# Performance work log

Hardware: AMD Instinct MI355X
Metric: run time of the kernel (lower is better)

The kernel has to match this reference:

```python
import jax, jax.numpy as jnp
import numpy as np

B, S, H, I, SI, E, TOPK = 2, 1024, 1024, 512, 2048, 8, 2


def setup_inputs() -> dict:
    key = jax.random.key(0)
    ks = jax.random.split(key, 8)
    w = 0.02
    return {
        "hidden_states": jax.random.normal(ks[0], (B, S, H), jnp.float32),
        "router_weight": jax.random.normal(ks[1], (E, H), jnp.float32) * w,
        "gate_up_proj": jax.random.normal(ks[2], (E, 2 * I, H), jnp.float32) * w,
        "down_proj": jax.random.normal(ks[3], (E, H, I), jnp.float32) * w,
        "shared_gate_w": jax.random.normal(ks[4], (SI, H), jnp.float32) * w,
        "shared_up_w": jax.random.normal(ks[5], (SI, H), jnp.float32) * w,
        "shared_down_w": jax.random.normal(ks[6], (H, SI), jnp.float32) * w,
        "shared_expert_gate_w": jax.random.normal(ks[7], (1, H), jnp.float32) * w,
    }


def reference(hidden_states, router_weight, gate_up_proj, down_proj,
              shared_gate_w, shared_up_w, shared_down_w, shared_expert_gate_w):
    b, s, h = hidden_states.shape
    x = hidden_states.reshape(-1, h)  # [T, H]

    # shared expert (SwiGLU)
    shared = (jax.nn.silu(x @ shared_gate_w.T) * (x @ shared_up_w.T)) @ shared_down_w.T  # [T, H]

    # top-k softmax router (softmax in fp32, renormalized top-k weights)
    logits = x @ router_weight.T  # [T, E]
    probs = jax.nn.softmax(logits.astype(jnp.float32), axis=-1)
    top_v, top_i = jax.lax.top_k(probs, TOPK)
    top_v = (top_v / jnp.sum(top_v, axis=-1, keepdims=True)).astype(logits.dtype)  # [T, K]

    # combine weights per (token, expert): sum over k of routing weight * one_hot
    cw = jnp.sum(jax.nn.one_hot(top_i, E, dtype=top_v.dtype) * top_v[..., None], axis=1)  # [T, E]

    # grouped-expert SwiGLU (dense compute, masked combine == gather/scatter math)
    gu = jnp.einsum('th,eih->eti', x, gate_up_proj)  # [E, T, 2I]
    gate, up = jnp.split(gu, 2, axis=-1)
    act = jax.nn.silu(gate) * up  # [E, T, I]
    per_expert = jnp.einsum('eti,ehi->eth', act, down_proj)  # [E, T, H]
    expert_out = jnp.einsum('eth,te->th', per_expert, cw)  # [T, H]

    out = expert_out + jax.nn.sigmoid(x @ shared_expert_gate_w.T) * shared
    return out.reshape(b, s, h)
```

## Files before the change

### kernel.cpp

```cpp
#include <hip/hip_runtime.h>

#define T_TOK 2048
#define H_DIM 1024
#define I_DIM 512
#define SI_DIM 2048
#define E_NUM 8
#define NSLOT 4096

typedef __attribute__((ext_vector_type(8))) short short8;
typedef __attribute__((ext_vector_type(4))) float floatx4;

__device__ inline unsigned short f2bf(float f) {
  unsigned u = __builtin_bit_cast(unsigned, f);
  u = (u + 0x7FFFu + ((u >> 16) & 1u)) >> 16;
  return (unsigned short)u;
}
__device__ inline float bf2f(unsigned short u) {
  return __builtin_bit_cast(float, (unsigned)u << 16);
}

__device__ inline void gl_lds16(const void* g, void* l) {
  __builtin_amdgcn_global_load_lds(
      (const __attribute__((address_space(1))) unsigned int*)g,
      (__attribute__((address_space(3))) unsigned int*)l, 16, 0, 0);
}

__global__ void cast_all(const float* __restrict__ s0, const float* __restrict__ s1,
                         const float* __restrict__ s2, const float* __restrict__ s3,
                         const float* __restrict__ s4, const float* __restrict__ s5,
                         unsigned short* __restrict__ d0, unsigned short* __restrict__ d1,
                         unsigned short* __restrict__ d2, unsigned short* __restrict__ d3,
                         unsigned short* __restrict__ d4, unsigned short* __restrict__ d5) {
  long g = (long)blockIdx.x * blockDim.x + threadIdx.x;
  const float* s;
  unsigned short* d;
  long off;
  if (g < 524288L)       { s = s0; d = d0; off = g; }
  else if (g < 2621440L) { s = s1; d = d1; off = g - 524288L; }
  else if (g < 3670016L) { s = s2; d = d2; off = g - 2621440L; }
  else if (g < 4194304L) { s = s3; d = d3; off = g - 3670016L; }
  else if (g < 4718592L) { s = s4; d = d4; off = g - 4194304L; }
  else                   { s = s5; d = d5; off = g - 4718592L; }
  float4 v = ((const float4*)s)[off];
  ushort4 o;
  o.x = f2bf(v.x); o.y = f2bf(v.y); o.z = f2bf(v.z); o.w = f2bf(v.w);
  ((ushort4*)d)[off] = o;
}

__global__ void router_kernel(const float* __restrict__ x,
                              const float* __restrict__ rw,
                              const float* __restrict__ segw,
                              int* __restrict__ top2,
                              float2* __restrict__ w01,
                              float* __restrict__ sg) {
  int t = blockIdx.x * 4 + (threadIdx.x >> 6);
  int lane = threadIdx.x & 63;
  const float* xt = x + (long)t * H_DIM;
  float xv[16];
#pragma unroll
  for (int j = 0; j < 16; ++j) xv[j] = xt[j * 64 + lane];
  float dots[9];
#pragma unroll
  for (int e = 0; e < 8; ++e) {
    const float* w = rw + e * H_DIM;
    float s = 0.f;
#pragma unroll
    for (int j = 0; j < 16; ++j) s += xv[j] * w[j * 64 + lane];
    dots[e] = s;
  }
  {
    float s = 0.f;
#pragma unroll
    for (int j = 0; j < 16; ++j) s += xv[j] * segw[j * 64 + lane];
    dots[8] = s;
  }
#pragma unroll
  for (int off = 32; off > 0; off >>= 1) {
#pragma unroll
    for (int e = 0; e < 9; ++e) dots[e] += __shfl_xor(dots[e], off, 64);
  }
  if (lane == 0) {
    int e0 = 0;
    for (int e = 1; e < 8; ++e)
      if (dots[e] > dots[e0]) e0 = e;
    int e1 = (e0 == 0) ? 1 : 0;
    for (int e = 0; e < 8; ++e)
      if (e != e0 && dots[e] > dots[e1]) e1 = e;
    float p1 = expf(dots[e1] - dots[e0]);
    float w0 = 1.f / (1.f + p1);
    float w1 = p1 / (1.f + p1);
    top2[t] = e0 | (e1 << 8);
    w01[t] = make_float2(w0, w1);
    sg[t] = 1.f / (1.f + expf(-dots[8]));
  }
}

__global__ __launch_bounds__(256) void build_lists(
    const int* __restrict__ top2, int* __restrict__ cnt, int* __restrict__ ebase,
    int* __restrict__ slot_token, int* __restrict__ tok_slot) {
  const int e = blockIdx.x;
  const int tid = threadIdx.x;
  const int lane = tid & 63, wid = tid >> 6;
  __shared__ int wsum[4], wbelow[4];
  const int base_t = tid * 8;
  int mk[8], kk[8];
  int c = 0, below = 0;
#pragma unroll
  for (int j = 0; j < 8; ++j) {
    int p = top2[base_t + j];
    int e0 = p & 0xFF, e1 = (p >> 8) & 0xFF;
    below += (e0 < e) + (e1 < e);
    int m = 0, k = 0;
    if (e0 == e) { m = 1; k = 0; }
    else if (e1 == e) { m = 1; k = 1; }
    mk[j] = m; kk[j] = k;
    c += m;
  }
  int inc = c;
#pragma unroll
  for (int off = 1; off < 64; off <<= 1) {
    int n = __shfl_up(inc, off, 64);
    if (lane >= off) inc += n;
  }
  int bsum = below;
#pragma unroll
  for (int off = 32; off > 0; off >>= 1) bsum += __shfl_xor(bsum, off, 64);
  if (lane == 63) wsum[wid] = inc;
  if (lane == 0) wbelow[wid] = bsum;
  __syncthreads();
  int woff = 0;
#pragma unroll
  for (int i = 0; i < 4; ++i)
    if (i < wid) woff += wsum[i];
  int baseE = wbelow[0] + wbelow[1] + wbelow[2] + wbelow[3];
  int pos = baseE + woff + inc - c;
#pragma unroll
  for (int j = 0; j < 8; ++j) {
    if (mk[j]) {
      slot_token[pos] = base_t + j;
      tok_slot[2 * (base_t + j) + kk[j]] = pos;
      pos++;
    }
  }
  if (tid == 255) cnt[e] = woff + inc;
  if (tid == 0) ebase[e] = baseE;
}

template <bool GATHER, int BM>
__device__ __forceinline__ void swiglu_body(
    char* smem, int bx, int by, int e,
    const unsigned short* __restrict__ A, const unsigned short* __restrict__ Bg,
    const unsigned short* __restrict__ Bu, unsigned short* __restrict__ Out,
    const int* __restrict__ slot_token, const int* __restrict__ cnt,
    const int* __restrict__ ebase, int N, int K, long estrideB) {
  const int BK = 32;
  const int MT = BM / 32;
  const int ACH = BM / 64;
  const int tid = threadIdx.x;
  const int lane = tid & 63;
  const int wid = tid >> 6;
  const int wm = wid & 1;
  const int wn = wid >> 1;
  const int m0 = by * BM;
  const int n0 = bx * 64;
  int Meff = 0, baseE = 0;
  if (GATHER) {
    Meff = cnt[e];
    if (m0 >= Meff) return;
    baseE = ebase[e];
  }
  const unsigned short* BgE = Bg + (long)e * estrideB;
  const unsigned short* BuE = Bu + (long)e * estrideB;

  unsigned short* As = (unsigned short*)smem;
  unsigned short* Bgs = As + 2 * BM * BK;
  unsigned short* Bus = Bgs + 2 * 64 * BK;

  const int lrow = lane >> 2;
  const int lcol = (((lane & 3) ^ ((lrow >> 1) & 3)) << 4);

  const char* aP[ACH];
#pragma unroll
  for (int i = 0; i < ACH; ++i) {
    int m = m0 + wid * (16 * ACH) + i * 16 + lrow;
    long row;
    if (GATHER) {
      int mm = (m < Meff - 1) ? m : (Meff - 1);
      row = slot_token[baseE + mm];
    } else {
      row = m;
    }
    aP[i] = (const char*)A + row * (long)(K * 2) + lcol;
  }
  int nb = n0 + wid * 16 + lrow;
  const char* bgP = (const char*)BgE + (long)nb * (K * 2) + lcol;
  const char* buP = (const char*)BuE + (long)nb * (K * 2) + lcol;

  floatx4 accG[MT][2], accU[MT][2];
  floatx4 zero = {0.f, 0.f, 0.f, 0.f};
#pragma unroll
  for (int i = 0; i < MT; ++i)
#pragma unroll
    for (int j = 0; j < 2; ++j) { accG[i][j] = zero; accU[i][j] = zero; }

  const int ar = lane & 15;
  const int aksw = (((lane >> 4) ^ ((ar >> 1) & 3)) << 3);

  auto stage = [&](int p, int k0) {
#pragma unroll
    for (int i = 0; i < ACH; ++i)
      gl_lds16(aP[i] + (long)k0 * 2, &As[p * BM * BK + (wid * 16 * ACH + i * 16) * BK]);
    gl_lds16(bgP + (long)k0 * 2, &Bgs[p * 64 * BK + (wid * 16) * BK]);
    gl_lds16(buP + (long)k0 * 2, &Bus[p * 64 * BK + (wid * 16) * BK]);
  };

  stage(0, 0);
  const int NI = K / BK;
  for (int i = 0; i < NI; ++i) {
    __syncthreads();
    if (i + 1 < NI) stage((i + 1) & 1, (i + 1) * BK);
    const unsigned short* Ab = &As[(i & 1) * BM * BK];
    const unsigned short* Gb = &Bgs[(i & 1) * 64 * BK];
    const unsigned short* Ub = &Bus[(i & 1) * 64 * BK];
    short8 af[MT], bgf[2], buf2[2];
#pragma unroll
    for (int tm = 0; tm < MT; ++tm)
      af[tm] = *(const short8*)&Ab[(wm * (BM / 2) + tm * 16 + ar) * BK + aksw];
#pragma unroll
    for (int tn = 0; tn < 2; ++tn) {
      bgf[tn] = *(const short8*)&Gb[(wn * 32 + tn * 16 + ar) * BK + aksw];
      buf2[tn] = *(const short8*)&Ub[(wn * 32 + tn * 16 + ar) * BK + aksw];
    }
#pragma unroll
    for (int tm = 0; tm < MT; ++tm)
#pragma unroll
      for (int tn = 0; tn < 2; ++tn) {
        accG[tm][tn] = __builtin_amdgcn_mfma_f32_16x16x32_bf16(af[tm], bgf[tn], accG[tm][tn], 0, 0, 0);
        accU[tm][tn] = __builtin_amdgcn_mfma_f32_16x16x32_bf16(af[tm], buf2[tn], accU[tm][tn], 0, 0, 0);
      }
  }

#pragma unroll
  for (int tm = 0; tm < MT; ++tm)
#pragma unroll
    for (int tn = 0; tn < 2; ++tn)
#pragma unroll
      for (int r = 0; r < 4; ++r) {
        int row = m0 + wm * (BM / 2) + tm * 16 + (lane >> 4) * 4 + r;
        int col = n0 + wn * 32 + tn * 16 + (lane & 15);
        if (!GATHER || row < Meff) {
          float g = accG[tm][tn][r];
          float u = accU[tm][tn][r];
          float act = g / (1.f + expf(-g)) * u;
          Out[(long)(baseE + row) * N + col] = f2bf(act);
        }
      }
}

__global__ __launch_bounds__(256, 2) void swiglu_fused(
    const unsigned short* __restrict__ xb, const unsigned short* __restrict__ sgate,
    const unsigned short* __restrict__ sup, unsigned short* __restrict__ act_s,
    const unsigned short* __restrict__ gup, unsigned short* __restrict__ act_e,
    const int* __restrict__ slot_token, const int* __restrict__ cnt,
    const int* __restrict__ ebase) {
  __shared__ __align__(16) char smem[32768];
  int bid = blockIdx.x;
  if (bid < 512) {
    swiglu_body<false, 128>(smem, bid & 31, bid >> 5, 0, xb, sgate, sup, act_s,
                            nullptr, nullptr, nullptr, SI_DIM, H_DIM, 0);
  } else {
    int b2 = bid - 512;
    int e = b2 >> 8;
    int rem = b2 & 255;
    swiglu_body<true, 64>(smem, rem & 7, rem >> 3, e, xb, gup,
                          gup + (long)I_DIM * H_DIM, act_e, slot_token, cnt,
                          ebase, I_DIM, H_DIM, (long)2 * I_DIM * H_DIM);
  }
}

template <int MODE>
__device__ __forceinline__ void down_body(
    char* smem, int bx, int by, int e,
    const unsigned short* __restrict__ A, const unsigned short* __restrict__ B,
    float* __restrict__ OutF, unsigned short* __restrict__ OutB,
    const float* __restrict__ sg, const int* __restrict__ ebase,
    const int* __restrict__ cnt, int N, int K, long estrideB) {
  const int BM = 64, BK = 32;
  const int tid = threadIdx.x;
  const int lane = tid & 63;
  const int wid = tid >> 6;
  const int wm = wid & 1;
  const int wn = wid >> 1;
  const int m0 = by * BM;
  const int n0 = bx * 64;
  int Meff = 0, baseE = 0;
  if (MODE == 1) {
    Meff = cnt[e];
    if (m0 >= Meff) return;
    baseE = ebase[e];
  }
  const unsigned short* BE = B + (long)e * estrideB;

  unsigned short* As = (unsigned short*)smem;
  unsigned short* Bs = As + 2 * 64 * BK;

  const int lrow = lane >> 2;
  const int lcol = (((lane & 3) ^ ((lrow >> 1) & 3)) << 4);

  int m = m0 + wid * 16 + lrow;
  long arow;
  if (MODE == 1) {
    int mm = (m < Meff - 1) ? m : (Meff - 1);
    arow = baseE + mm;
  } else {
    arow = m;
  }
  const char* aP = (const char*)A + arow * (long)(K * 2) + lcol;
  int nb = n0 + wid * 16 + lrow;
  const char* bP = (const char*)BE + (long)nb * (K * 2) + lcol;

  floatx4 acc[2][2];
  floatx4 zero = {0.f, 0.f, 0.f, 0.f};
#pragma unroll
  for (int i = 0; i < 2; ++i)
#pragma unroll
    for (int j = 0; j < 2; ++j) acc[i][j] = zero;

  const int ar = lane & 15;
  const int aksw = (((lane >> 4) ^ ((ar >> 1) & 3)) << 3);

  auto stage = [&](int p, int k0) {
    gl_lds16(aP + (long)k0 * 2, &As[p * 64 * BK + (wid * 16) * BK]);
    gl_lds16(bP + (long)k0 * 2, &Bs[p * 64 * BK + (wid * 16) * BK]);
  };

  stage(0, 0);
  const int NI = K / BK;
  for (int i = 0; i < NI; ++i) {
    __syncthreads();
    if (i + 1 < NI) stage((i + 1) & 1, (i + 1) * BK);
    const unsigned short* Ab = &As[(i & 1) * 64 * BK];
    const unsigned short* Bb = &Bs[(i & 1) * 64 * BK];
    short8 af[2], bf[2];
#pragma unroll
    for (int tm = 0; tm < 2; ++tm)
      af[tm] = *(const short8*)&Ab[(wm * 32 + tm * 16 + ar) * BK + aksw];
#pragma unroll
    for (int tn = 0; tn < 2; ++tn)
      bf[tn] = *(const short8*)&Bb[(wn * 32 + tn * 16 + ar) * BK + aksw];
#pragma unroll
    for (int tm = 0; tm < 2; ++tm)
#pragma unroll
      for (int tn = 0; tn < 2; ++tn)
        acc[tm][tn] = __builtin_amdgcn_mfma_f32_16x16x32_bf16(af[tm], bf[tn], acc[tm][tn], 0, 0, 0);
  }

#pragma unroll
  for (int tm = 0; tm < 2; ++tm)
#pragma unroll
    for (int r = 0; r < 4; ++r) {
      int row = m0 + wm * 32 + tm * 16 + (lane >> 4) * 4 + r;
#pragma unroll
      for (int tn = 0; tn < 2; ++tn) {
        int col = n0 + wn * 32 + tn * 16 + (lane & 15);
        float v = acc[tm][tn][r];
        if (MODE == 0) {
          OutF[(long)row * N + col] = sg[row] * v;
        } else if (row < Meff) {
          OutB[(long)(baseE + row) * N + col] = f2bf(v);
        }
      }
    }
}

__global__ __launch_bounds__(256, 4) void down_fused(
    const unsigned short* __restrict__ act_s, const unsigned short* __restrict__ sdown,
    float* __restrict__ out, const float* __restrict__ sg,
    const unsigned short* __restrict__ act_e, const unsigned short* __restrict__ downw,
    unsigned short* __restrict__ eout, const int* __restrict__ ebase,
    const int* __restrict__ cnt) {
  __shared__ __align__(16) char smem[16384];
  int bid = blockIdx.x;
  if (bid < 512) {
    down_body<0>(smem, bid & 15, bid >> 4, 0, act_s, sdown, out, nullptr, sg,
                 nullptr, nullptr, H_DIM, SI_DIM, 0);
  } else {
    int b2 = bid - 512;
    int e = b2 >> 9;
    int rem = b2 & 511;
    down_body<1>(smem, rem & 15, rem >> 4, e, act_e, downw, nullptr, eout,
                 nullptr, ebase, cnt, H_DIM, I_DIM, (long)H_DIM * I_DIM);
  }
}

__global__ __launch_bounds__(256) void combine_kernel(
    float* __restrict__ out, const unsigned short* __restrict__ eout,
    const float2* __restrict__ w01, const int* __restrict__ tok_slot) {
  int t = blockIdx.x;
  int c = threadIdx.x;
  float2 wr = w01[t];
  int s0 = tok_slot[2 * t];
  int s1 = tok_slot[2 * t + 1];
  ushort4 e0 = ((const ushort4*)(eout + (long)s0 * H_DIM))[c];
  ushort4 e1 = ((const ushort4*)(eout + (long)s1 * H_DIM))[c];
  float4* op = &((float4*)(out + (long)t * H_DIM))[c];
  float4 o = *op;
  o.x += wr.x * bf2f(e0.x) + wr.y * bf2f(e1.x);
  o.y += wr.x * bf2f(e0.y) + wr.y * bf2f(e1.y);
  o.z += wr.x * bf2f(e0.z) + wr.y * bf2f(e1.z);
  o.w += wr.x * bf2f(e0.w) + wr.y * bf2f(e1.w);
  *op = o;
}

extern "C" void kernel_launch(void* const* d_in, const int* in_sizes, int n_in,
                              void* d_out, int out_size, void* d_ws, size_t ws_size,
                              hipStream_t stream) {
  const float* x = (const float*)d_in[0];
  const float* rw = (const float*)d_in[1];
  const float* gup = (const float*)d_in[2];
  const float* dwn = (const float*)d_in[3];
  const float* sgw = (const float*)d_in[4];
  const float* suw = (const float*)d_in[5];
  const float* sdw = (const float*)d_in[6];
  const float* segw = (const float*)d_in[7];
  float* out = (float*)d_out;

  char* w = (char*)d_ws;
  unsigned short* xb = (unsigned short*)(w + 0);
  unsigned short* gup_b = (unsigned short*)(w + 4194304L);
  unsigned short* down_b = (unsigned short*)(w + 20971520L);
  unsigned short* sgate_b = (unsigned short*)(w + 29360128L);
  unsigned short* sup_b = (unsigned short*)(w + 33554432L);
  unsigned short* sdown_b = (unsigned short*)(w + 37748736L);
  unsigned short* act_s = (unsigned short*)(w + 41943040L);
  unsigned short* act_e = (unsigned short*)(w + 50331648L);
  unsigned short* eout = (unsigned short*)(w + 54525952L);
  float* sg = (float*)(w + 62914560L);
  int* top2 = (int*)(w + 62922752L);
  float2* w01 = (float2*)(w + 62930944L);
  int* cnt = (int*)(w + 62947328L);
  int* ebase = (int*)(w + 62947584L);
  int* slot_token = (int*)(w + 62947840L);
  int* tok_slot = (int*)(w + 62964224L);

  cast_all<<<20480, 256, 0, stream>>>(x, gup, dwn, sgw, suw, sdw, xb, gup_b,
                                      down_b, sgate_b, sup_b, sdown_b);
  router_kernel<<<512, 256, 0, stream>>>(x, rw, segw, top2, w01, sg);
  build_lists<<<E_NUM, 256, 0, stream>>>(top2, cnt, ebase, slot_token, tok_slot);
  swiglu_fused<<<2560, 256, 0, stream>>>(xb, sgate_b, sup_b, act_s, gup_b,
                                         act_e, slot_token, cnt, ebase);
  down_fused<<<4608, 256, 0, stream>>>(act_s, sdown_b, out, sg, act_e, down_b,
                                       eout, ebase, cnt);
  combine_kernel<<<T_TOK, 256, 0, stream>>>(out, eout, w01, tok_slot);
}
```

Baseline: 218.0 us.

## Merge cast and router kernels, enlarge GEMM tiles, split-K shared down projection

Merges the weight/activation cast and router into one launch, removing a kernel boundary. Grows the expert gate/up tile to 128 rows and the down-projection tile to 128x128, giving fewer blocks and more reuse per LDS load. The shared down GEMM is split in K into two halves: one writes fp32 into the output and the other writes a bf16 partial into the reused x buffer. Combine then sums the halves and applies the sigmoid gate. The larger tiles raise register pressure and lower occupancy (launch bounds drop to 2), and the bf16 partial adds a rounding step.

```diff
diff --git a/kernel.cpp b/kernel.cpp
--- a/kernel.cpp
+++ b/kernel.cpp
@@ -25,73 +25,71 @@
       (__attribute__((address_space(3))) unsigned int*)l, 16, 0, 0);
 }
 
-__global__ void cast_all(const float* __restrict__ s0, const float* __restrict__ s1,
-                         const float* __restrict__ s2, const float* __restrict__ s3,
-                         const float* __restrict__ s4, const float* __restrict__ s5,
-                         unsigned short* __restrict__ d0, unsigned short* __restrict__ d1,
-                         unsigned short* __restrict__ d2, unsigned short* __restrict__ d3,
-                         unsigned short* __restrict__ d4, unsigned short* __restrict__ d5) {
-  long g = (long)blockIdx.x * blockDim.x + threadIdx.x;
-  const float* s;
-  unsigned short* d;
-  long off;
-  if (g < 524288L)       { s = s0; d = d0; off = g; }
-  else if (g < 2621440L) { s = s1; d = d1; off = g - 524288L; }
-  else if (g < 3670016L) { s = s2; d = d2; off = g - 2621440L; }
-  else if (g < 4194304L) { s = s3; d = d3; off = g - 3670016L; }
-  else if (g < 4718592L) { s = s4; d = d4; off = g - 4194304L; }
-  else                   { s = s5; d = d5; off = g - 4718592L; }
-  float4 v = ((const float4*)s)[off];
-  ushort4 o;
-  o.x = f2bf(v.x); o.y = f2bf(v.y); o.z = f2bf(v.z); o.w = f2bf(v.w);
-  ((ushort4*)d)[off] = o;
-}
-
-__global__ void router_kernel(const float* __restrict__ x,
-                              const float* __restrict__ rw,
-                              const float* __restrict__ segw,
-                              int* __restrict__ top2,
-                              float2* __restrict__ w01,
-                              float* __restrict__ sg) {
-  int t = blockIdx.x * 4 + (threadIdx.x >> 6);
-  int lane = threadIdx.x & 63;
-  const float* xt = x + (long)t * H_DIM;
-  float xv[16];
-#pragma unroll
-  for (int j = 0; j < 16; ++j) xv[j] = xt[j * 64 + lane];
-  float dots[9];
-#pragma unroll
-  for (int e = 0; e < 8; ++e) {
-    const float* w = rw + e * H_DIM;
-    float s = 0.f;
-#pragma unroll
-    for (int j = 0; j < 16; ++j) s += xv[j] * w[j * 64 + lane];
-    dots[e] = s;
-  }
-  {
-    float s = 0.f;
-#pragma unroll
-    for (int j = 0; j < 16; ++j) s += xv[j] * segw[j * 64 + lane];
-    dots[8] = s;
-  }
-#pragma unroll
-  for (int off = 32; off > 0; off >>= 1) {
-#pragma unroll
-    for (int e = 0; e < 9; ++e) dots[e] += __shfl_xor(dots[e], off, 64);
-  }
-  if (lane == 0) {
-    int e0 = 0;
-    for (int e = 1; e < 8; ++e)
-      if (dots[e] > dots[e0]) e0 = e;
-    int e1 = (e0 == 0) ? 1 : 0;
-    for (int e = 0; e < 8; ++e)
-      if (e != e0 && dots[e] > dots[e1]) e1 = e;
-    float p1 = expf(dots[e1] - dots[e0]);
-    float w0 = 1.f / (1.f + p1);
-    float w1 = p1 / (1.f + p1);
-    top2[t] = e0 | (e1 << 8);
-    w01[t] = make_float2(w0, w1);
-    sg[t] = 1.f / (1.f + expf(-dots[8]));
+__global__ __launch_bounds__(256) void cast_router(
+    const float* __restrict__ x, const float* __restrict__ rw,
+    const float* __restrict__ segw,
+    const float* __restrict__ s1, const float* __restrict__ s2,
+    const float* __restrict__ s3, const float* __restrict__ s4,
+    const float* __restrict__ s5,
+    unsigned short* __restrict__ d0, unsigned short* __restrict__ d1,
+    unsigned short* __restrict__ d2, unsigned short* __restrict__ d3,
+    unsigned short* __restrict__ d4, unsigned short* __restrict__ d5,
+    int* __restrict__ top2, float2* __restrict__ w01, float* __restrict__ sg) {
+  const int bid = blockIdx.x;
+  if (bid < 512) {
+    int t = bid * 4 + (threadIdx.x >> 6);
+    int lane = threadIdx.x & 63;
+    const float* xt = x + (long)t * H_DIM;
+    float xv[16];
+#pragma unroll
+    for (int j = 0; j < 16; ++j) xv[j] = xt[j * 64 + lane];
+    float dots[9];
+#pragma unroll
+    for (int e = 0; e < 8; ++e) {
+      const float* w = rw + e * H_DIM;
+      float s = 0.f;
+#pragma unroll
+      for (int j = 0; j < 16; ++j) s += xv[j] * w[j * 64 + lane];
+      dots[e] = s;
+    }
+    {
+      float s = 0.f;
+#pragma unroll
+      for (int j = 0; j < 16; ++j) s += xv[j] * segw[j * 64 + lane];
+      dots[8] = s;
+    }
+#pragma unroll
+    for (int off = 32; off > 0; off >>= 1) {
+#pragma unroll
+      for (int e = 0; e < 9; ++e) dots[e] += __shfl_xor(dots[e], off, 64);
+    }
+    if (lane == 0) {
+      int e0 = 0;
+      for (int e = 1; e < 8; ++e)
+        if (dots[e] > dots[e0]) e0 = e;
+      int e1 = (e0 == 0) ? 1 : 0;
+      for (int e = 0; e < 8; ++e)
+        if (e != e0 && dots[e] > dots[e1]) e1 = e;
+      float p1 = expf(dots[e1] - dots[e0]);
+      top2[t] = e0 | (e1 << 8);
+      w01[t] = make_float2(1.f / (1.f + p1), p1 / (1.f + p1));
+      sg[t] = 1.f / (1.f + expf(-dots[8]));
+    }
+  } else {
+    long g = (long)(bid - 512) * 256 + threadIdx.x;
+    const float* s;
+    unsigned short* d;
+    long off;
+    if (g < 524288L)       { s = x;  d = d0; off = g; }
+    else if (g < 2621440L) { s = s1; d = d1; off = g - 524288L; }
+    else if (g < 3670016L) { s = s2; d = d2; off = g - 2621440L; }
+    else if (g < 4194304L) { s = s3; d = d3; off = g - 3670016L; }
+    else if (g < 4718592L) { s = s4; d = d4; off = g - 4194304L; }
+    else                   { s = s5; d = d5; off = g - 4718592L; }
+    float4 v = ((const float4*)s)[off];
+    ushort4 o;
+    o.x = f2bf(v.x); o.y = f2bf(v.y); o.z = f2bf(v.z); o.w = f2bf(v.w);
+    ((ushort4*)d)[off] = o;
   }
 }
 
@@ -146,16 +144,14 @@
   if (tid == 0) ebase[e] = baseE;
 }
 
-template <bool GATHER, int BM>
+template <bool GATHER>
 __device__ __forceinline__ void swiglu_body(
     char* smem, int bx, int by, int e,
     const unsigned short* __restrict__ A, const unsigned short* __restrict__ Bg,
     const unsigned short* __restrict__ Bu, unsigned short* __restrict__ Out,
     const int* __restrict__ slot_token, const int* __restrict__ cnt,
     const int* __restrict__ ebase, int N, int K, long estrideB) {
-  const int BK = 32;
-  const int MT = BM / 32;
-  const int ACH = BM / 64;
+  const int BM = 128, BK = 32;
   const int tid = threadIdx.x;
   const int lane = tid & 63;
   const int wid = tid >> 6;
@@ -179,10 +175,10 @@
   const int lrow = lane >> 2;
   const int lcol = (((lane & 3) ^ ((lrow >> 1) & 3)) << 4);
 
-  const char* aP[ACH];
-#pragma unroll
-  for (int i = 0; i < ACH; ++i) {
-    int m = m0 + wid * (16 * ACH) + i * 16 + lrow;
+  const char* aP[2];
+#pragma unroll
+  for (int i = 0; i < 2; ++i) {
+    int m = m0 + wid * 32 + i * 16 + lrow;
     long row;
     if (GATHER) {
       int mm = (m < Meff - 1) ? m : (Meff - 1);
@@ -196,10 +192,10 @@
   const char* bgP = (const char*)BgE + (long)nb * (K * 2) + lcol;
   const char* buP = (const char*)BuE + (long)nb * (K * 2) + lcol;
 
-  floatx4 accG[MT][2], accU[MT][2];
+  floatx4 accG[4][2], accU[4][2];
   floatx4 zero = {0.f, 0.f, 0.f, 0.f};
 #pragma unroll
-  for (int i = 0; i < MT; ++i)
+  for (int i = 0; i < 4; ++i)
 #pragma unroll
     for (int j = 0; j < 2; ++j) { accG[i][j] = zero; accU[i][j] = zero; }
 
@@ -208,8 +204,8 @@
 
   auto stage = [&](int p, int k0) {
 #pragma unroll
-    for (int i = 0; i < ACH; ++i)
-      gl_lds16(aP[i] + (long)k0 * 2, &As[p * BM * BK + (wid * 16 * ACH + i * 16) * BK]);
+    for (int i = 0; i < 2; ++i)
+      gl_lds16(aP[i] + (long)k0 * 2, &As[p * BM * BK + (wid * 32 + i * 16) * BK]);
     gl_lds16(bgP + (long)k0 * 2, &Bgs[p * 64 * BK + (wid * 16) * BK]);
     gl_lds16(buP + (long)k0 * 2, &Bus[p * 64 * BK + (wid * 16) * BK]);
   };
@@ -222,17 +218,17 @@
     const unsigned short* Ab = &As[(i & 1) * BM * BK];
     const unsigned short* Gb = &Bgs[(i & 1) * 64 * BK];
     const unsigned short* Ub = &Bus[(i & 1) * 64 * BK];
-    short8 af[MT], bgf[2], buf2[2];
-#pragma unroll
-    for (int tm = 0; tm < MT; ++tm)
-      af[tm] = *(const short8*)&Ab[(wm * (BM / 2) + tm * 16 + ar) * BK + aksw];
+    short8 af[4], bgf[2], buf2[2];
+#pragma unroll
+    for (int tm = 0; tm < 4; ++tm)
+      af[tm] = *(const short8*)&Ab[(wm * 64 + tm * 16 + ar) * BK + aksw];
 #pragma unroll
     for (int tn = 0; tn < 2; ++tn) {
       bgf[tn] = *(const short8*)&Gb[(wn * 32 + tn * 16 + ar) * BK + aksw];
       buf2[tn] = *(const short8*)&Ub[(wn * 32 + tn * 16 + ar) * BK + aksw];
     }
 #pragma unroll
-    for (int tm = 0; tm < MT; ++tm)
+    for (int tm = 0; tm < 4; ++tm)
 #pragma unroll
       for (int tn = 0; tn < 2; ++tn) {
         accG[tm][tn] = __builtin_amdgcn_mfma_f32_16x16x32_bf16(af[tm], bgf[tn], accG[tm][tn], 0, 0, 0);
@@ -241,12 +237,12 @@
   }
 
 #pragma unroll
-  for (int tm = 0; tm < MT; ++tm)
+  for (int tm = 0; tm < 4; ++tm)
 #pragma unroll
     for (int tn = 0; tn < 2; ++tn)
 #pragma unroll
       for (int r = 0; r < 4; ++r) {
-        int row = m0 + wm * (BM / 2) + tm * 16 + (lane >> 4) * 4 + r;
+        int row = m0 + wm * 64 + tm * 16 + (lane >> 4) * 4 + r;
         int col = n0 + wn * 32 + tn * 16 + (lane & 15);
         if (!GATHER || row < Meff) {
           float g = accG[tm][tn][r];
@@ -266,15 +262,15 @@
   __shared__ __align__(16) char smem[32768];
   int bid = blockIdx.x;
   if (bid < 512) {
-    swiglu_body<false, 128>(smem, bid & 31, bid >> 5, 0, xb, sgate, sup, act_s,
-                            nullptr, nullptr, nullptr, SI_DIM, H_DIM, 0);
+    swiglu_body<false>(smem, bid & 31, bid >> 5, 0, xb, sgate, sup, act_s,
+                       nullptr, nullptr, nullptr, SI_DIM, H_DIM, 0);
   } else {
     int b2 = bid - 512;
-    int e = b2 >> 8;
-    int rem = b2 & 255;
-    swiglu_body<true, 64>(smem, rem & 7, rem >> 3, e, xb, gup,
-                          gup + (long)I_DIM * H_DIM, act_e, slot_token, cnt,
-                          ebase, I_DIM, H_DIM, (long)2 * I_DIM * H_DIM);
+    int e = b2 >> 7;
+    int rem = b2 & 127;
+    swiglu_body<true>(smem, rem & 7, rem >> 3, e, xb, gup,
+                      gup + (long)I_DIM * H_DIM, act_e, slot_token, cnt,
+                      ebase, I_DIM, H_DIM, (long)2 * I_DIM * H_DIM);
   }
 }
 
@@ -283,16 +279,16 @@
     char* smem, int bx, int by, int e,
     const unsigned short* __restrict__ A, const unsigned short* __restrict__ B,
     float* __restrict__ OutF, unsigned short* __restrict__ OutB,
-    const float* __restrict__ sg, const int* __restrict__ ebase,
-    const int* __restrict__ cnt, int N, int K, long estrideB) {
-  const int BM = 64, BK = 32;
+    const int* __restrict__ ebase, const int* __restrict__ cnt,
+    int N, int Kstride, int kbeg, int kcnt, long estrideB) {
+  const int BM = 128, BK = 32;
   const int tid = threadIdx.x;
   const int lane = tid & 63;
   const int wid = tid >> 6;
   const int wm = wid & 1;
   const int wn = wid >> 1;
   const int m0 = by * BM;
-  const int n0 = bx * 64;
+  const int n0 = bx * 128;
   int Meff = 0, baseE = 0;
   if (MODE == 1) {
     Meff = cnt[e];
@@ -302,70 +298,80 @@
   const unsigned short* BE = B + (long)e * estrideB;
 
   unsigned short* As = (unsigned short*)smem;
-  unsigned short* Bs = As + 2 * 64 * BK;
+  unsigned short* Bs = As + 2 * BM * BK;
 
   const int lrow = lane >> 2;
   const int lcol = (((lane & 3) ^ ((lrow >> 1) & 3)) << 4);
 
-  int m = m0 + wid * 16 + lrow;
-  long arow;
-  if (MODE == 1) {
-    int mm = (m < Meff - 1) ? m : (Meff - 1);
-    arow = baseE + mm;
-  } else {
-    arow = m;
-  }
-  const char* aP = (const char*)A + arow * (long)(K * 2) + lcol;
-  int nb = n0 + wid * 16 + lrow;
-  const char* bP = (const char*)BE + (long)nb * (K * 2) + lcol;
-
-  floatx4 acc[2][2];
+  const char* aP[2];
+  const char* bP[2];
+#pragma unroll
+  for (int i = 0; i < 2; ++i) {
+    int m = m0 + wid * 32 + i * 16 + lrow;
+    long arow;
+    if (MODE == 1) {
+      int mm = (m < Meff - 1) ? m : (Meff - 1);
+      arow = baseE + mm;
+    } else {
+      arow = m;
+    }
+    aP[i] = (const char*)A + arow * (long)(Kstride * 2) + (long)kbeg * 2 + lcol;
+    int n = n0 + wid * 32 + i * 16 + lrow;
+    bP[i] = (const char*)BE + (long)n * (Kstride * 2) + (long)kbeg * 2 + lcol;
+  }
+
+  floatx4 acc[4][4];
   floatx4 zero = {0.f, 0.f, 0.f, 0.f};
 #pragma unroll
-  for (int i = 0; i < 2; ++i)
-#pragma unroll
-    for (int j = 0; j < 2; ++j) acc[i][j] = zero;
+  for (int i = 0; i < 4; ++i)
+#pragma unroll
+    for (int j = 0; j < 4; ++j) acc[i][j] = zero;
 
   const int ar = lane & 15;
   const int aksw = (((lane >> 4) ^ ((ar >> 1) & 3)) << 3);
 
   auto stage = [&](int p, int k0) {
-    gl_lds16(aP + (long)k0 * 2, &As[p * 64 * BK + (wid * 16) * BK]);
-    gl_lds16(bP + (long)k0 * 2, &Bs[p * 64 * BK + (wid * 16) * BK]);
+#pragma unroll
+    for (int i = 0; i < 2; ++i) {
+      gl_lds16(aP[i] + (long)k0 * 2, &As[p * BM * BK + (wid * 32 + i * 16) * BK]);
+      gl_lds16(bP[i] + (long)k0 * 2, &Bs[p * BM * BK + (wid * 32 + i * 16) * BK]);
+    }
   };
 
   stage(0, 0);
-  const int NI = K / BK;
+  const int NI = kcnt / BK;
   for (int i = 0; i < NI; ++i) {
     __syncthreads();
     if (i + 1 < NI) stage((i + 1) & 1, (i + 1) * BK);
-    const unsigned short* Ab = &As[(i & 1) * 64 * BK];
-    const unsigned short* Bb = &Bs[(i & 1) * 64 * BK];
-    short8 af[2], bf[2];
-#pragma unroll
-    for (int tm = 0; tm < 2; ++tm)
-      af[tm] = *(const short8*)&Ab[(wm * 32 + tm * 16 + ar) * BK + aksw];
-#pragma unroll
-    for (int tn = 0; tn < 2; ++tn)
-      bf[tn] = *(const short8*)&Bb[(wn * 32 + tn * 16 + ar) * BK + aksw];
-#pragma unroll
-    for (int tm = 0; tm < 2; ++tm)
-#pragma unroll
-      for (int tn = 0; tn < 2; ++tn)
+    const unsigned short* Ab = &As[(i & 1) * BM * BK];
+    const unsigned short* Bb = &Bs[(i & 1) * BM * BK];
+    short8 af[4], bf[4];
+#pragma unroll
+    for (int tm = 0; tm < 4; ++tm)
+      af[tm] = *(const short8*)&Ab[(wm * 64 + tm * 16 + ar) * BK + aksw];
+#pragma unroll
+    for (int tn = 0; tn < 4; ++tn)
+      bf[tn] = *(const short8*)&Bb[(wn * 64 + tn * 16 + ar) * BK + aksw];
+#pragma unroll
+    for (int tm = 0; tm < 4; ++tm)
+#pragma unroll
+      for (int tn = 0; tn < 4; ++tn)
         acc[tm][tn] = __builtin_amdgcn_mfma_f32_16x16x32_bf16(af[tm], bf[tn], acc[tm][tn], 0, 0, 0);
   }
 
 #pragma unroll
-  for (int tm = 0; tm < 2; ++tm)
+  for (int tm = 0; tm < 4; ++tm)
 #pragma unroll
     for (int r = 0; r < 4; ++r) {
-      int row = m0 + wm * 32 + tm * 16 + (lane >> 4) * 4 + r;
-#pragma unroll
-      for (int tn = 0; tn < 2; ++tn) {
-        int col = n0 + wn * 32 + tn * 16 + (lane & 15);
+      int row = m0 + wm * 64 + tm * 16 + (lane >> 4) * 4 + r;
+#pragma unroll
+      for (int tn = 0; tn < 4; ++tn) {
+        int col = n0 + wn * 64 + tn * 16 + (lane & 15);
         float v = acc[tm][tn][r];
         if (MODE == 0) {
-          OutF[(long)row * N + col] = sg[row] * v;
+          OutF[(long)row * N + col] = v;
+        } else if (MODE == 2) {
+          OutB[(long)row * N + col] = f2bf(v);
         } else if (row < Meff) {
           OutB[(long)(baseE + row) * N + col] = f2bf(v);
         }
@@ -373,42 +379,49 @@
     }
 }
 
-__global__ __launch_bounds__(256, 4) void down_fused(
+__global__ __launch_bounds__(256, 2) void down_fused(
     const unsigned short* __restrict__ act_s, const unsigned short* __restrict__ sdown,
-    float* __restrict__ out, const float* __restrict__ sg,
+    float* __restrict__ out, unsigned short* __restrict__ spart,
     const unsigned short* __restrict__ act_e, const unsigned short* __restrict__ downw,
     unsigned short* __restrict__ eout, const int* __restrict__ ebase,
     const int* __restrict__ cnt) {
-  __shared__ __align__(16) char smem[16384];
+  __shared__ __align__(16) char smem[32768];
   int bid = blockIdx.x;
-  if (bid < 512) {
-    down_body<0>(smem, bid & 15, bid >> 4, 0, act_s, sdown, out, nullptr, sg,
-                 nullptr, nullptr, H_DIM, SI_DIM, 0);
+  if (bid < 128) {
+    down_body<0>(smem, bid & 7, bid >> 3, 0, act_s, sdown, out, nullptr,
+                 nullptr, nullptr, H_DIM, SI_DIM, 0, 1024, 0);
+  } else if (bid < 256) {
+    int b = bid - 128;
+    down_body<2>(smem, b & 7, b >> 3, 0, act_s, sdown, nullptr, spart,
+                 nullptr, nullptr, H_DIM, SI_DIM, 1024, 1024, 0);
   } else {
-    int b2 = bid - 512;
-    int e = b2 >> 9;
-    int rem = b2 & 511;
-    down_body<1>(smem, rem & 15, rem >> 4, e, act_e, downw, nullptr, eout,
-                 nullptr, ebase, cnt, H_DIM, I_DIM, (long)H_DIM * I_DIM);
+    int b2 = bid - 256;
+    int e = b2 >> 7;
+    int rem = b2 & 127;
+    down_body<1>(smem, rem & 7, rem >> 3, e, act_e, downw, nullptr, eout,
+                 ebase, cnt, H_DIM, I_DIM, 0, I_DIM, (long)H_DIM * I_DIM);
   }
 }
 
 __global__ __launch_bounds__(256) void combine_kernel(
-    float* __restrict__ out, const unsigned short* __restrict__ eout,
+    float* __restrict__ out, const unsigned short* __restrict__ spart,
+    const unsigned short* __restrict__ eout, const float* __restrict__ sg,
     const float2* __restrict__ w01, const int* __restrict__ tok_slot) {
   int t = blockIdx.x;
   int c = threadIdx.x;
+  float sgr = sg[t];
   float2 wr = w01[t];
   int s0 = tok_slot[2 * t];
   int s1 = tok_slot[2 * t + 1];
+  ushort4 p1 = ((const ushort4*)(spart + (long)t * H_DIM))[c];
   ushort4 e0 = ((const ushort4*)(eout + (long)s0 * H_DIM))[c];
   ushort4 e1 = ((const ushort4*)(eout + (long)s1 * H_DIM))[c];
   float4* op = &((float4*)(out + (long)t * H_DIM))[c];
   float4 o = *op;
-  o.x += wr.x * bf2f(e0.x) + wr.y * bf2f(e1.x);
-  o.y += wr.x * bf2f(e0.y) + wr.y * bf2f(e1.y);
-  o.z += wr.x * bf2f(e0.z) + wr.y * bf2f(e1.z);
-  o.w += wr.x * bf2f(e0.w) + wr.y * bf2f(e1.w);
+  o.x = sgr * (o.x + bf2f(p1.x)) + wr.x * bf2f(e0.x) + wr.y * bf2f(e1.x);
+  o.y = sgr * (o.y + bf2f(p1.y)) + wr.x * bf2f(e0.y) + wr.y * bf2f(e1.y);
+  o.z = sgr * (o.z + bf2f(p1.z)) + wr.x * bf2f(e0.z) + wr.y * bf2f(e1.z);
+  o.w = sgr * (o.w + bf2f(p1.w)) + wr.x * bf2f(e0.w) + wr.y * bf2f(e1.w);
   *op = o;
 }
 
@@ -442,14 +455,15 @@
   int* ebase = (int*)(w + 62947584L);
   int* slot_token = (int*)(w + 62947840L);
   int* tok_slot = (int*)(w + 62964224L);
-
-  cast_all<<<20480, 256, 0, stream>>>(x, gup, dwn, sgw, suw, sdw, xb, gup_b,
-                                      down_b, sgate_b, sup_b, sdown_b);
-  router_kernel<<<512, 256, 0, stream>>>(x, rw, segw, top2, w01, sg);
+  unsigned short* spart = xb;
+
+  cast_router<<<20992, 256, 0, stream>>>(x, rw, segw, gup, dwn, sgw, suw, sdw,
+                                         xb, gup_b, down_b, sgate_b, sup_b,
+                                         sdown_b, top2, w01, sg);
   build_lists<<<E_NUM, 256, 0, stream>>>(top2, cnt, ebase, slot_token, tok_slot);
-  swiglu_fused<<<2560, 256, 0, stream>>>(xb, sgate_b, sup_b, act_s, gup_b,
+  swiglu_fused<<<1536, 256, 0, stream>>>(xb, sgate_b, sup_b, act_s, gup_b,
                                          act_e, slot_token, cnt, ebase);
-  down_fused<<<4608, 256, 0, stream>>>(act_s, sdown_b, out, sg, act_e, down_b,
-                                       eout, ebase, cnt);
-  combine_kernel<<<T_TOK, 256, 0, stream>>>(out, eout, w01, tok_slot);
-}
+  down_fused<<<1280, 256, 0, stream>>>(act_s, sdown_b, out, spart, act_e,
+                                       down_b, eout, ebase, cnt);
+  combine_kernel<<<T_TOK, 256, 0, stream>>>(out, spart, eout, sg, w01, tok_slot);
+}
```

Measured after the change: 208.4 us. 1.05x faster.
